# Performance work log

Measured on AMD Instinct MI355X. Metric: run time of the kernel, lower is better.

The kernel has to match this reference:

```python
import jax, jax.numpy as jnp
import numpy as np

NUM_HEADS = 4

def setup_inputs() -> dict:
    key = jax.random.key(0)
    ks = jax.random.split(key, 8)
    B, L, D, Lc = 4, 4096, 256, 4096
    s = 0.02
    return {
        "x": jax.random.normal(ks[0], (B, L, D), jnp.float32),
        "context": jax.random.normal(ks[1], (B, Lc, D), jnp.float32),
        "Wq": jax.random.normal(ks[2], (D, D), jnp.float32) * s,
        "bq": jax.random.normal(ks[3], (D,), jnp.float32) * s,
        "Wkv": jax.random.normal(ks[4], (D, 2 * D), jnp.float32) * s,
        "bkv": jax.random.normal(ks[5], (2 * D,), jnp.float32) * s,
        "Wp": jax.random.normal(ks[6], (D, D), jnp.float32) * s,
        "bp": jax.random.normal(ks[7], (D,), jnp.float32) * s,
    }


def reference(x, context, Wq, bq, Wkv, bkv, Wp, bp):
    B, L, D = x.shape
    Hn = NUM_HEADS
    hd = D // Hn
    Hs = Ws = int(L ** 0.5)
    scale = hd ** (-0.5)

    # projections
    q = (x @ Wq + bq).reshape(B, L, Hn, hd).transpose(0, 2, 1, 3)        # [B,H,L,hd]
    kv = (context @ Wkv + bkv).reshape(B, -1, 2, Hn, hd)
    k = kv[:, :, 0].transpose(0, 2, 1, 3)                                 # [B,H,Lc,hd]
    v = kv[:, :, 1].transpose(0, 2, 1, 3)                                 # [B,H,Lc,hd]

    attn = jnp.einsum('bhqd,bhkd->bhqk', q, k) * scale                    # [B,H,L,Lc]
    attn_weights = jax.nn.softmax(attn, axis=-1)

    attn_map = attn_weights.mean(axis=1).sum(axis=-1).reshape(B, Hs, Ws)  # [B,H,W]

    out = jnp.einsum('bhqk,bhkd->bhqd', attn_weights, v)                  # [B,H,L,hd]
    out = out.transpose(0, 2, 1, 3).reshape(B, L, D)
    out = out @ Wp + bp
    return (out + x, attn_map)
```

## Files before the change

### kernel.cpp

```cpp
#include <hip/hip_runtime.h>
#include <stdint.h>

typedef unsigned short u16;
typedef short s16x8 __attribute__((ext_vector_type(8)));
typedef u16   u16x8 __attribute__((ext_vector_type(8)));
typedef float f32x4 __attribute__((ext_vector_type(4)));
typedef float f32x16 __attribute__((ext_vector_type(16)));

#define QSCALE 0.180336880111169f

__device__ __forceinline__ u16 f2bf(float f) {
  union { float f; uint32_t u; } v; v.f = f;
  uint32_t r = (v.u + 0x7fffu + ((v.u >> 16) & 1u)) >> 16;
  return (u16)r;
}

__device__ __forceinline__ f32x4 mfma16(s16x8 a, s16x8 b, f32x4 c) {
  return __builtin_amdgcn_mfma_f32_16x16x32_bf16(a, b, c, 0, 0, 0);
}
__device__ __forceinline__ f32x16 mfma32(s16x8 a, s16x8 b, f32x16 c) {
  return __builtin_amdgcn_mfma_f32_32x32x16_bf16(a, b, c, 0, 0, 0);
}

__device__ __forceinline__ void gload16(const void* g, void* l) {
  __builtin_amdgcn_global_load_lds(
      (const __attribute__((address_space(1))) void*)g,
      (__attribute__((address_space(3))) void*)l, 16, 0, 0);
}

__device__ __forceinline__ s16x8 ldsr(const u16* base, int row, int colb) {
  return *(const s16x8*)((const char*)base + row * 128 + (colb ^ ((row & 7) << 4)));
}

__device__ __forceinline__ uint32_t cvtpk(float lo, float hi) {
  uint32_t r;
  asm("v_cvt_pk_bf16_f32 %0, %1, %2" : "=v"(r) : "v"(lo), "v"(hi));
  return r;
}
__device__ __forceinline__ void hswap(uint32_t& a, uint32_t& b) {
  asm("v_permlane32_swap_b32 %0, %1" : "+v"(a), "+v"(b));
}
__device__ __forceinline__ float cross_sum(float v) {
  float t = v, u = v;
  asm("v_permlane32_swap_b32 %0, %1" : "+v"(t), "+v"(u));
  return t + u;
}

__global__ void k_convert(const float* __restrict__ x, const float* __restrict__ ctx,
                          const float* __restrict__ wq, const float* __restrict__ wkv,
                          const float* __restrict__ wp,
                          u16* __restrict__ xb, u16* __restrict__ cb,
                          u16* __restrict__ wqT, u16* __restrict__ wkvT,
                          u16* __restrict__ wpT, float* __restrict__ amap) {
  int tid = blockIdx.x * 256 + threadIdx.x;
  if (tid < 2097152) {
    const float* src; u16* dst; int off;
    if (tid < 1048576) { src = x;   dst = xb; off = tid * 4; }
    else               { src = ctx; dst = cb; off = (tid - 1048576) * 4; }
    f32x4 v = *(const f32x4*)(src + off);
    u16* d = dst + off;
    d[0] = f2bf(v.x); d[1] = f2bf(v.y); d[2] = f2bf(v.z); d[3] = f2bf(v.w);
    if (tid < 16384) amap[tid] = 1.0f;
  } else {
    int t4 = (tid - 2097152) * 4;
#pragma unroll
    for (int j = 0; j < 4; j++) {
      int t = t4 + j;
      if (t < 65536) {
        int k = t >> 8, n = t & 255;
        wqT[n * 256 + k] = f2bf(wq[t]);
      } else if (t < 196608) {
        int t2 = t - 65536;
        int k = t2 >> 9, n = t2 & 511;
        wkvT[n * 256 + k] = f2bf(wkv[t2]);
      } else {
        int t2 = t - 196608;
        int k = t2 >> 8, n = t2 & 255;
        wpT[n * 256 + k] = f2bf(wp[t2]);
      }
    }
  }
}

template<int EPI>
__global__ __launch_bounds__(256, 2) void k_gemm(
    const u16* __restrict__ A, const u16* __restrict__ Bt,
    const float* __restrict__ bias, const float* __restrict__ xres,
    u16* __restrict__ o16a, u16* __restrict__ o16b, float* __restrict__ o32) {
  __shared__ u16 Als[2][128 * 64];
  __shared__ u16 Bls[2][64 * 64];
  const int m0 = blockIdx.x * 128;
  const int n0 = blockIdx.y * 64;
  const int tid = threadIdx.x, w = tid >> 6, l = tid & 63;
  const int lr = l & 15, lg = l >> 4;
  const int wm = (w >> 1) * 64, wn = (w & 1) * 32;

  auto stage = [&](int buf, int k0) {
    const char* sa = (const char*)A;
#pragma unroll
    for (int i = 0; i < 4; i++) {
      int dbase = (w * 4 + i) * 1024;
      int d = dbase + l * 16;
      int row = d >> 7, colb = d & 127;
      gload16(sa + (size_t)(m0 + row) * 512 + k0 * 2 + (colb ^ ((row & 7) << 4)),
              (char*)Als[buf] + dbase);
    }
    const char* sb = (const char*)Bt;
#pragma unroll
    for (int i = 0; i < 2; i++) {
      int dbase = (w * 2 + i) * 1024;
      int d = dbase + l * 16;
      int row = d >> 7, colb = d & 127;
      gload16(sb + (size_t)(n0 + row) * 512 + k0 * 2 + (colb ^ ((row & 7) << 4)),
              (char*)Bls[buf] + dbase);
    }
  };

  f32x4 acc[4][2];
#pragma unroll
  for (int i = 0; i < 4; i++)
#pragma unroll
    for (int j = 0; j < 2; j++) acc[i][j] = (f32x4){0.f, 0.f, 0.f, 0.f};

  stage(0, 0);
  __syncthreads();
  int cur = 0;
  for (int ks = 0; ks < 4; ks++) {
    if (ks < 3) stage(cur ^ 1, (ks + 1) * 64);
    s16x8 a[4][2], b[2][2];
#pragma unroll
    for (int mt = 0; mt < 4; mt++)
#pragma unroll
      for (int kf = 0; kf < 2; kf++)
        a[mt][kf] = ldsr(Als[cur], wm + mt * 16 + lr, lg * 16 + kf * 64);
#pragma unroll
    for (int nt = 0; nt < 2; nt++)
#pragma unroll
      for (int kf = 0; kf < 2; kf++)
        b[nt][kf] = ldsr(Bls[cur], wn + nt * 16 + lr, lg * 16 + kf * 64);
#pragma unroll
    for (int mt = 0; mt < 4; mt++)
#pragma unroll
      for (int nt = 0; nt < 2; nt++) {
        acc[mt][nt] = mfma16(a[mt][0], b[nt][0], acc[mt][nt]);
        acc[mt][nt] = mfma16(a[mt][1], b[nt][1], acc[mt][nt]);
      }
    __syncthreads();
    cur ^= 1;
  }

#pragma unroll
  for (int mt = 0; mt < 4; mt++)
#pragma unroll
    for (int nt = 0; nt < 2; nt++)
#pragma unroll
      for (int r = 0; r < 4; r++) {
        int gm = m0 + wm + mt * 16 + lg * 4 + r;
        int gn = n0 + wn + nt * 16 + lr;
        float val = acc[mt][nt][r] + bias[gn];
        if constexpr (EPI == 0) {
          int b_ = gm >> 12, ql = gm & 4095, h = gn >> 6, dd = gn & 63;
          o16a[(((size_t)(b_ * 4 + h) * 4096 + ql) << 6) + dd] = f2bf(val * QSCALE);
        } else if constexpr (EPI == 1) {
          int b_ = gm >> 12, ql = gm & 4095;
          int s = gn >> 8, inner = gn & 255, h = inner >> 6, dd = inner & 63;
          if (s) {
            size_t addr = (((size_t)(b_ * 4 + h) * 64 + (ql >> 6)) * 64 + dd) * 64 + (ql & 63);
            o16b[addr] = f2bf(val);
          } else {
            size_t addr = (((size_t)(b_ * 4 + h) * 4096 + ql) << 6) + dd;
            o16a[addr] = f2bf(val);
          }
        } else {
          size_t idx = (size_t)gm * 256 + gn;
          o32[idx] = val + xres[idx];
        }
      }
}

__global__ __launch_bounds__(256, 4) void k_flash(
    const u16* __restrict__ qb, const u16* __restrict__ kb,
    const u16* __restrict__ vtb, u16* __restrict__ ob) {
  __shared__ char smem[33024];
  u16* kls0 = (u16*)(smem);
  u16* kls1 = (u16*)(smem + 8192);
  u16* vls0 = (u16*)(smem + 16384);
  u16* vls1 = (u16*)(smem + 24576);
  float* comb = (float*)smem;
  float* lsb  = (float*)(smem + 32768);
  const int id = blockIdx.y * 32 + blockIdx.x;
  const int sw = (id & 7) * 128 + (id >> 3);
  const int bh = sw >> 6;
  const int q0 = (sw & 63) * 64;
  const int tid = threadIdx.x, w = tid >> 6, l = tid & 63;
  const int lr32 = l & 31, hi = l >> 5;
  const int qh = w & 1, kvh = w >> 1;
  const char* kbase  = (const char*)(kb + (size_t)bh * 262144);
  const char* vtbase = (const char*)(vtb + (size_t)bh * 262144);

  s16x8 qf[4];
  {
    const u16* qp = qb + ((size_t)bh * 4096 + q0 + qh * 32 + lr32) * 64 + hi * 8;
#pragma unroll
    for (int mm = 0; mm < 4; mm++) qf[mm] = *(const s16x8*)(qp + mm * 16);
  }

  auto stage = [&](u16* kbuf, u16* vbuf, int t) {
    const char* ks = kbase  + (size_t)t * 8192;
    const char* vs = vtbase + (size_t)t * 8192;
    int dbase = w * 2048 + (l >> 6) * 1024;
#pragma unroll
    for (int i = 0; i < 2; i++) {
      int d = w * 2048 + i * 1024 + l * 16;
      int row = d >> 7, colb = d & 127;
      int so = row * 128 + (colb ^ ((row & 7) << 4));
      gload16(ks + so, (char*)kbuf + d);
      gload16(vs + so, (char*)vbuf + d);
    }
    (void)dbase;
  };

  f32x16 o0, o1;
  float lsum = 0.f;
#pragma unroll
  for (int r = 0; r < 16; r++) { o0[r] = 0.f; o1[r] = 0.f; }

  auto compute = [&](const u16* kc, const u16* vc) {
    s16x8 kf[4];
#pragma unroll
    for (int mm = 0; mm < 4; mm++)
      kf[mm] = ldsr(kc, kvh * 32 + lr32, mm * 32 + 16 * hi);
    f32x16 s;
#pragma unroll
    for (int r = 0; r < 16; r++) s[r] = 0.f;
    __builtin_amdgcn_s_setprio(1);
#pragma unroll
    for (int mm = 0; mm < 4; mm++) s = mfma32(kf[mm], qf[mm], s);
    __builtin_amdgcn_s_setprio(0);
#pragma unroll
    for (int r = 0; r < 16; r++) s[r] = __builtin_amdgcn_exp2f(s[r]);
    float acc = 0.f;
#pragma unroll
    for (int r = 0; r < 16; r++) acc += s[r];
    lsum += acc;
#pragma unroll
    for (int ks2 = 0; ks2 < 2; ks2++) {
      uint32_t A0 = cvtpk(s[8 * ks2 + 0], s[8 * ks2 + 1]);
      uint32_t A1 = cvtpk(s[8 * ks2 + 2], s[8 * ks2 + 3]);
      uint32_t B0 = cvtpk(s[8 * ks2 + 4], s[8 * ks2 + 5]);
      uint32_t B1 = cvtpk(s[8 * ks2 + 6], s[8 * ks2 + 7]);
      hswap(A0, B0);
      hswap(A1, B1);
      union { uint32_t wv[4]; s16x8 h; } pa;
      pa.wv[0] = A0; pa.wv[1] = A1; pa.wv[2] = B0; pa.wv[3] = B1;
      int vcol = kvh * 64 + 32 * ks2 + 16 * hi;
      s16x8 v0 = ldsr(vc, lr32,      vcol);
      s16x8 v1 = ldsr(vc, 32 + lr32, vcol);
      __builtin_amdgcn_s_setprio(1);
      o0 = mfma32(pa.h, v0, o0);
      o1 = mfma32(pa.h, v1, o1);
      __builtin_amdgcn_s_setprio(0);
    }
  };

  stage(kls0, vls0, 0);
#pragma unroll 1
  for (int tt = 0; tt < 32; tt++) {
    const int t = tt * 2;
    asm volatile("s_waitcnt vmcnt(0)" ::: "memory");
    __builtin_amdgcn_s_barrier();
    asm volatile("" ::: "memory");
    stage(kls1, vls1, t + 1);
    compute(kls0, vls0);
    asm volatile("s_waitcnt vmcnt(0)" ::: "memory");
    __builtin_amdgcn_s_barrier();
    asm volatile("" ::: "memory");
    if (t + 2 < 64) stage(kls0, vls0, t + 2);
    compute(kls1, vls1);
  }

  float ltot = cross_sum(lsum);
  __syncthreads();
  if (kvh == 1) {
    float* cp = comb + ((size_t)qh * 64 + l) * 33;
#pragma unroll
    for (int r = 0; r < 16; r++) { cp[r] = o0[r]; cp[16 + r] = o1[r]; }
    cp[32] = ltot;
  }
  __syncthreads();
  if (kvh == 0) {
    const float* cp = comb + ((size_t)qh * 64 + l) * 33;
#pragma unroll
    for (int r = 0; r < 16; r++) { o0[r] += cp[r]; o1[r] += cp[16 + r]; }
    ltot += cp[32];
    lsb[qh * 32 + lr32] = ltot;
    const int b_ = bh >> 2, h = bh & 3;
    u16* obase = ob + (size_t)b_ * 4096 * 256 + h * 64;
#pragma unroll
    for (int r = 0; r < 16; r++) {
      int crow = (r & 3) + 8 * (r >> 2) + 4 * hi;
      float inv = __builtin_amdgcn_rcpf(lsb[qh * 32 + crow]);
      size_t qrow = (size_t)(q0 + qh * 32 + crow);
      obase[qrow * 256 + lr32]      = f2bf(o0[r] * inv);
      obase[qrow * 256 + 32 + lr32] = f2bf(o1[r] * inv);
    }
  }
}

extern "C" void kernel_launch(void* const* d_in, const int* in_sizes, int n_in,
                              void* d_out, int out_size, void* d_ws, size_t ws_size,
                              hipStream_t stream) {
  const float* x   = (const float*)d_in[0];
  const float* ctx = (const float*)d_in[1];
  const float* Wq  = (const float*)d_in[2];
  const float* bq  = (const float*)d_in[3];
  const float* Wkv = (const float*)d_in[4];
  const float* bkv = (const float*)d_in[5];
  const float* Wp  = (const float*)d_in[6];
  const float* bp  = (const float*)d_in[7];

  char* ws = (char*)d_ws;
  u16* xb    = (u16*)(ws);
  u16* cb    = (u16*)(ws + 8388608);
  u16* wqT   = (u16*)(ws + 16777216);
  u16* wkvT  = (u16*)(ws + 16908288);
  u16* wpT   = (u16*)(ws + 17170432);
  u16* qbuf  = (u16*)(ws + 17301504);
  u16* kbuf  = (u16*)(ws + 25690112);
  u16* vtbuf = (u16*)(ws + 34078720);
  u16* aout  = (u16*)(ws + 42467328);
  float* out  = (float*)d_out;
  float* amap = out + 4194304;

  k_convert<<<8448, 256, 0, stream>>>(x, ctx, Wq, Wkv, Wp, xb, cb, wqT, wkvT, wpT, amap);
  k_gemm<0><<<dim3(128, 4), 256, 0, stream>>>(xb, wqT, bq, nullptr, qbuf, nullptr, nullptr);
  k_gemm<1><<<dim3(128, 8), 256, 0, stream>>>(cb, wkvT, bkv, nullptr, kbuf, vtbuf, nullptr);
  k_flash<<<dim3(32, 32), 256, 0, stream>>>(qbuf, kbuf, vtbuf, aout);
  k_gemm<2><<<dim3(128, 4), 256, 0, stream>>>(aout, wpT, bp, x, nullptr, nullptr, out);
}
```

Before: 136.9 us.

## Double query tile per flash block to reuse K/V LDS tiles across two Q subtiles

Each flash-attention block now processes 128 queries instead of 64, with every wave holding two 32-row Q fragments that share the same K and V fragments loaded from LDS. This halves the number of blocks and the total global K/V traffic and LDS reads per query, and raises the MFMA work per loaded tile. In exchange, accumulator registers double, launch bounds drop to 2 waves per SIMD, and only 512 blocks remain, which lowers occupancy and latency hiding. The cross-wave combine buffer and the normalisation store are widened to match.

```diff
diff --git a/kernel.cpp b/kernel.cpp
--- a/kernel.cpp
+++ b/kernel.cpp
@@ -178,37 +178,39 @@
       }
 }
 
-__global__ __launch_bounds__(256, 4) void k_flash(
+__global__ __launch_bounds__(256, 2) void k_flash(
     const u16* __restrict__ qb, const u16* __restrict__ kb,
     const u16* __restrict__ vtb, u16* __restrict__ ob) {
-  __shared__ char smem[33024];
+  __shared__ char smem[34304];
   u16* kls0 = (u16*)(smem);
   u16* kls1 = (u16*)(smem + 8192);
   u16* vls0 = (u16*)(smem + 16384);
   u16* vls1 = (u16*)(smem + 24576);
   float* comb = (float*)smem;
-  float* lsb  = (float*)(smem + 32768);
+  float* lsb  = (float*)(smem + 33792);
   const int id = blockIdx.y * 32 + blockIdx.x;
-  const int sw = (id & 7) * 128 + (id >> 3);
-  const int bh = sw >> 6;
-  const int q0 = (sw & 63) * 64;
+  const int sw = (id & 7) * 64 + (id >> 3);
+  const int bh = sw >> 5;
+  const int q0 = (sw & 31) * 128;
   const int tid = threadIdx.x, w = tid >> 6, l = tid & 63;
   const int lr32 = l & 31, hi = l >> 5;
-  const int qh = w & 1, kvh = w >> 1;
+  const int qq = w & 1, kvh = w >> 1;
   const char* kbase  = (const char*)(kb + (size_t)bh * 262144);
   const char* vtbase = (const char*)(vtb + (size_t)bh * 262144);
 
-  s16x8 qf[4];
+  s16x8 qfA[4], qfB[4];
   {
-    const u16* qp = qb + ((size_t)bh * 4096 + q0 + qh * 32 + lr32) * 64 + hi * 8;
-#pragma unroll
-    for (int mm = 0; mm < 4; mm++) qf[mm] = *(const s16x8*)(qp + mm * 16);
+    const u16* qp = qb + ((size_t)bh * 4096 + q0 + qq * 64 + lr32) * 64 + hi * 8;
+#pragma unroll
+    for (int mm = 0; mm < 4; mm++) {
+      qfA[mm] = *(const s16x8*)(qp + mm * 16);
+      qfB[mm] = *(const s16x8*)(qp + 2048 + mm * 16);
+    }
   }
 
   auto stage = [&](u16* kbuf, u16* vbuf, int t) {
     const char* ks = kbase  + (size_t)t * 8192;
     const char* vs = vtbase + (size_t)t * 8192;
-    int dbase = w * 2048 + (l >> 6) * 1024;
 #pragma unroll
     for (int i = 0; i < 2; i++) {
       int d = w * 2048 + i * 1024 + l * 16;
@@ -217,48 +219,67 @@
       gload16(ks + so, (char*)kbuf + d);
       gload16(vs + so, (char*)vbuf + d);
     }
-    (void)dbase;
   };
 
-  f32x16 o0, o1;
-  float lsum = 0.f;
-#pragma unroll
-  for (int r = 0; r < 16; r++) { o0[r] = 0.f; o1[r] = 0.f; }
+  f32x16 oA0, oA1, oB0, oB1;
+  float lsA = 0.f, lsB = 0.f;
+#pragma unroll
+  for (int r = 0; r < 16; r++) { oA0[r] = 0.f; oA1[r] = 0.f; oB0[r] = 0.f; oB1[r] = 0.f; }
 
   auto compute = [&](const u16* kc, const u16* vc) {
     s16x8 kf[4];
 #pragma unroll
     for (int mm = 0; mm < 4; mm++)
       kf[mm] = ldsr(kc, kvh * 32 + lr32, mm * 32 + 16 * hi);
-    f32x16 s;
-#pragma unroll
-    for (int r = 0; r < 16; r++) s[r] = 0.f;
+    f32x16 sA, sB;
+#pragma unroll
+    for (int r = 0; r < 16; r++) { sA[r] = 0.f; sB[r] = 0.f; }
     __builtin_amdgcn_s_setprio(1);
 #pragma unroll
-    for (int mm = 0; mm < 4; mm++) s = mfma32(kf[mm], qf[mm], s);
+    for (int mm = 0; mm < 4; mm++) {
+      sA = mfma32(kf[mm], qfA[mm], sA);
+      sB = mfma32(kf[mm], qfB[mm], sB);
+    }
     __builtin_amdgcn_s_setprio(0);
 #pragma unroll
-    for (int r = 0; r < 16; r++) s[r] = __builtin_amdgcn_exp2f(s[r]);
-    float acc = 0.f;
-#pragma unroll
-    for (int r = 0; r < 16; r++) acc += s[r];
-    lsum += acc;
+    for (int r = 0; r < 16; r++) {
+      sA[r] = __builtin_amdgcn_exp2f(sA[r]);
+      sB[r] = __builtin_amdgcn_exp2f(sB[r]);
+    }
+    float aA = 0.f, aB = 0.f;
+#pragma unroll
+    for (int r = 0; r < 16; r++) { aA += sA[r]; aB += sB[r]; }
+    lsA += aA; lsB += aB;
+    s16x8 vf[2][2];
 #pragma unroll
     for (int ks2 = 0; ks2 < 2; ks2++) {
-      uint32_t A0 = cvtpk(s[8 * ks2 + 0], s[8 * ks2 + 1]);
-      uint32_t A1 = cvtpk(s[8 * ks2 + 2], s[8 * ks2 + 3]);
-      uint32_t B0 = cvtpk(s[8 * ks2 + 4], s[8 * ks2 + 5]);
-      uint32_t B1 = cvtpk(s[8 * ks2 + 6], s[8 * ks2 + 7]);
+      int vcol = kvh * 64 + 32 * ks2 + 16 * hi;
+      vf[ks2][0] = ldsr(vc, lr32,      vcol);
+      vf[ks2][1] = ldsr(vc, 32 + lr32, vcol);
+    }
+#pragma unroll
+    for (int ks2 = 0; ks2 < 2; ks2++) {
+      uint32_t A0 = cvtpk(sA[8 * ks2 + 0], sA[8 * ks2 + 1]);
+      uint32_t A1 = cvtpk(sA[8 * ks2 + 2], sA[8 * ks2 + 3]);
+      uint32_t B0 = cvtpk(sA[8 * ks2 + 4], sA[8 * ks2 + 5]);
+      uint32_t B1 = cvtpk(sA[8 * ks2 + 6], sA[8 * ks2 + 7]);
       hswap(A0, B0);
       hswap(A1, B1);
       union { uint32_t wv[4]; s16x8 h; } pa;
       pa.wv[0] = A0; pa.wv[1] = A1; pa.wv[2] = B0; pa.wv[3] = B1;
-      int vcol = kvh * 64 + 32 * ks2 + 16 * hi;
-      s16x8 v0 = ldsr(vc, lr32,      vcol);
-      s16x8 v1 = ldsr(vc, 32 + lr32, vcol);
+      uint32_t C0 = cvtpk(sB[8 * ks2 + 0], sB[8 * ks2 + 1]);
+      uint32_t C1 = cvtpk(sB[8 * ks2 + 2], sB[8 * ks2 + 3]);
+      uint32_t D0 = cvtpk(sB[8 * ks2 + 4], sB[8 * ks2 + 5]);
+      uint32_t D1 = cvtpk(sB[8 * ks2 + 6], sB[8 * ks2 + 7]);
+      hswap(C0, D0);
+      hswap(C1, D1);
+      union { uint32_t wv[4]; s16x8 h; } pb;
+      pb.wv[0] = C0; pb.wv[1] = C1; pb.wv[2] = D0; pb.wv[3] = D1;
       __builtin_amdgcn_s_setprio(1);
-      o0 = mfma32(pa.h, v0, o0);
-      o1 = mfma32(pa.h, v1, o1);
+      oA0 = mfma32(pa.h, vf[ks2][0], oA0);
+      oA1 = mfma32(pa.h, vf[ks2][1], oA1);
+      oB0 = mfma32(pb.h, vf[ks2][0], oB0);
+      oB1 = mfma32(pb.h, vf[ks2][1], oB1);
       __builtin_amdgcn_s_setprio(0);
     }
   };
@@ -279,30 +300,42 @@
     compute(kls1, vls1);
   }
 
-  float ltot = cross_sum(lsum);
+  float ltA = cross_sum(lsA);
+  float ltB = cross_sum(lsB);
   __syncthreads();
   if (kvh == 1) {
-    float* cp = comb + ((size_t)qh * 64 + l) * 33;
-#pragma unroll
-    for (int r = 0; r < 16; r++) { cp[r] = o0[r]; cp[16 + r] = o1[r]; }
-    cp[32] = ltot;
+    float* cp = comb + ((size_t)qq * 64 + l) * 66;
+#pragma unroll
+    for (int r = 0; r < 16; r++) {
+      cp[r] = oA0[r]; cp[16 + r] = oA1[r];
+      cp[32 + r] = oB0[r]; cp[48 + r] = oB1[r];
+    }
+    cp[64] = ltA; cp[65] = ltB;
   }
   __syncthreads();
   if (kvh == 0) {
-    const float* cp = comb + ((size_t)qh * 64 + l) * 33;
-#pragma unroll
-    for (int r = 0; r < 16; r++) { o0[r] += cp[r]; o1[r] += cp[16 + r]; }
-    ltot += cp[32];
-    lsb[qh * 32 + lr32] = ltot;
+    const float* cp = comb + ((size_t)qq * 64 + l) * 66;
+#pragma unroll
+    for (int r = 0; r < 16; r++) {
+      oA0[r] += cp[r]; oA1[r] += cp[16 + r];
+      oB0[r] += cp[32 + r]; oB1[r] += cp[48 + r];
+    }
+    ltA += cp[64]; ltB += cp[65];
+    lsb[qq * 64 + lr32]      = ltA;
+    lsb[qq * 64 + 32 + lr32] = ltB;
     const int b_ = bh >> 2, h = bh & 3;
     u16* obase = ob + (size_t)b_ * 4096 * 256 + h * 64;
 #pragma unroll
     for (int r = 0; r < 16; r++) {
       int crow = (r & 3) + 8 * (r >> 2) + 4 * hi;
-      float inv = __builtin_amdgcn_rcpf(lsb[qh * 32 + crow]);
-      size_t qrow = (size_t)(q0 + qh * 32 + crow);
-      obase[qrow * 256 + lr32]      = f2bf(o0[r] * inv);
-      obase[qrow * 256 + 32 + lr32] = f2bf(o1[r] * inv);
+      float invA = __builtin_amdgcn_rcpf(lsb[qq * 64 + crow]);
+      float invB = __builtin_amdgcn_rcpf(lsb[qq * 64 + 32 + crow]);
+      size_t qrA = (size_t)(q0 + qq * 64 + crow);
+      size_t qrB = qrA + 32;
+      obase[qrA * 256 + lr32]      = f2bf(oA0[r] * invA);
+      obase[qrA * 256 + 32 + lr32] = f2bf(oA1[r] * invA);
+      obase[qrB * 256 + lr32]      = f2bf(oB0[r] * invB);
+      obase[qrB * 256 + 32 + lr32] = f2bf(oB1[r] * invB);
     }
   }
 }
@@ -335,6 +368,6 @@
   k_convert<<<8448, 256, 0, stream>>>(x, ctx, Wq, Wkv, Wp, xb, cb, wqT, wkvT, wpT, amap);
   k_gemm<0><<<dim3(128, 4), 256, 0, stream>>>(xb, wqT, bq, nullptr, qbuf, nullptr, nullptr);
   k_gemm<1><<<dim3(128, 8), 256, 0, stream>>>(cb, wkvT, bkv, nullptr, kbuf, vtbuf, nullptr);
-  k_flash<<<dim3(32, 32), 256, 0, stream>>>(qbuf, kbuf, vtbuf, aout);
+  k_flash<<<dim3(32, 16), 256, 0, stream>>>(qbuf, kbuf, vtbuf, aout);
   k_gemm<2><<<dim3(128, 4), 256, 0, stream>>>(aout, wpT, bp, x, nullptr, nullptr, out);
 }
```

New measurement: 127.6 us. -6.7%, faster.
